# Optimization experiments

Measured on AMD Instinct MI355X. Metric: run time of the kernel, lower is better.

## Reference

```python
import jax, jax.numpy as jnp
import numpy as np

B, L, R, H, TE = 4, 256, 64, 768, 100
TH = 0.5  # all four thresholds default to 0.5


def extract_first_embeddings(tok, start_probs, end_probs, threshold):
    """For each token i with start_prob>th, pair it with the nearest end index j>=i
    with end_prob>th; span embedding = mean(tok[i:j+1]). Valid spans are packed
    (in order) into a [b, l, h] table padded with zeros, with a [b, l] validity mask.
    Vectorized, jit-friendly reconstruction of the repo's span extractor."""
    b, l, h = tok.shape
    ar = jnp.arange(l)
    starts = start_probs > threshold            # [b, l]
    ends = end_probs > threshold                # [b, l]
    end_pos = jnp.where(ends, ar[None, :], l)   # l = sentinel 'no end'
    next_end = jax.lax.cummin(end_pos, axis=1, reverse=True)  # first end >= i
    valid = starts & (next_end < l)             # [b, l]
    j = jnp.minimum(next_end, l - 1)
    # inclusive span mean via prefix sums: mean = (csum[j+1] - csum[i]) / (j-i+1)
    csum0 = jnp.concatenate([jnp.zeros((b, 1, h), tok.dtype), jnp.cumsum(tok, axis=1)], axis=1)
    upper = jnp.take_along_axis(csum0, (j + 1)[:, :, None], axis=1)  # [b, l, h]
    lower = csum0[:, :-1]                                             # csum0[:, i]
    span_len = (j - ar[None, :] + 1).astype(tok.dtype)[:, :, None]
    span_emb = (upper - lower) / span_len
    # pack valid spans to the front (pad_sequence-style), pad with zeros to length l
    rank = jnp.cumsum(valid, axis=1) - 1
    rank_safe = jnp.where(valid, rank, l)       # dump invalids into extra slot l
    padded = jnp.zeros((b, l + 1, h), tok.dtype).at[
        jnp.arange(b)[:, None], rank_safe
    ].set(jnp.where(valid[:, :, None], span_emb, 0.0))[:, :l]
    num = valid.sum(axis=1)
    mask = ar[None, :] < num[:, None]
    return padded, mask


def setup_inputs() -> dict:
    key = jax.random.key(0)
    ks = jax.random.split(key, 12)
    s = 0.02
    return {
        "embs": jax.random.normal(ks[0], (B, L, H), jnp.float32),
        "h_gs": jax.random.normal(ks[1], (B, H), jnp.float32),
        "rel_embs": jax.random.normal(ks[2], (R, H), jnp.float32),
        "rel_transe_embs": jax.random.normal(ks[3], (R, TE), jnp.float32),
        "fc_w": jax.random.normal(ks[4], (8, H), jnp.float32) * s,
        "fc_b": jax.random.normal(ks[5], (8,), jnp.float32) * s,
        "Wm": jax.random.normal(ks[6], (10, H, H), jnp.float32) * s,
        "Wb": jax.random.normal(ks[7], (10, H), jnp.float32) * s,
        "V_w": jax.random.normal(ks[8], (H,), jnp.float32) * s,
        "V_b": jax.random.normal(ks[9], (1,), jnp.float32) * s,
        "rproj_w": jax.random.normal(ks[10], (TE, H), jnp.float32) * s,
        "rproj_b": jax.random.normal(ks[11], (H,), jnp.float32) * s,
    }


def _forward(embs, h_gs, rel_embs, rel_transe_embs, fc_w, fc_b, Wm, Wb, V_w, V_b, rproj_w, rproj_b):
    sig = jax.nn.sigmoid
    b_rel = rel_transe_embs @ rproj_w + rproj_b            # [r, h] r_proj

    # ---- first-stage scalar heads on tokens ----
    f_sub_s = embs @ fc_w[0] + fc_b[0]                     # [b, l]
    f_sub_e = embs @ fc_w[1] + fc_b[1]
    b_obj_s = embs @ fc_w[2] + fc_b[2]
    b_obj_e = embs @ fc_w[3] + fc_b[3]

    f_pad, f_mask = extract_first_embeddings(embs, sig(f_sub_s), sig(f_sub_e), TH)
    b_pad, b_mask = extract_first_embeddings(embs, sig(b_obj_s), sig(b_obj_e), TH)
    f_s_w = (f_pad @ Wm[0] + Wb[0]) * f_mask[:, :, None].astype(embs.dtype)  # f_W_s
    b_o_w = (b_pad @ Wm[1] + Wb[1]) * b_mask[:, :, None].astype(embs.dtype)  # b_W_s

    # ---- relation attention: tanh(W_r rel + W_g hg + W_x tok), broadcast [b,l,r,h] ----
    def rel_attn(rel, iWr, iWg, iWx):
        relp = rel @ Wm[iWr] + Wb[iWr]                     # [r, h]
        hgp = h_gs @ Wm[iWg] + Wb[iWg]                     # [b, h]
        tokp = embs @ Wm[iWx] + Wb[iWx]                    # [b, l, h]
        e = jnp.tanh(tokp[:, :, None, :] + relp[None, None, :, :] + hgp[:, None, None, :])
        v = e @ V_w + V_b                                  # [b, l, r]
        A = jax.nn.softmax(v, axis=1)                      # softmax over tokens
        C = jnp.einsum('blr,blh->brh', A, embs)            # relation context
        return C

    f_C = rel_attn(rel_embs, 2, 3, 4)
    b_C = rel_attn(b_rel, 5, 6, 7)

    # ---- pairwise table heads; Hijk = Hik[:,:,None]+C[:,None]+tok[:,:,None] is linear
    # under the scalar head, so compute logits without materializing [b,l,r,h] ----
    f_Hik = f_s_w + embs @ Wm[8] + Wb[8]                   # [b, l, h] (f_Wx2)
    b_Hik = b_o_w + embs @ Wm[9] + Wb[9]                   # (b_Wx2)

    def pair_logits(Hik, C, i):
        t = (Hik + embs) @ fc_w[i]                         # [b, l]
        return t[:, :, None] + (C @ fc_w[i])[:, None, :] + fc_b[i]  # [b, l, r]

    f_obj_s = pair_logits(f_Hik, f_C, 4)
    f_obj_e = pair_logits(f_Hik, f_C, 5)
    b_sub_s = pair_logits(b_Hik, b_C, 6)
    b_sub_e = pair_logits(b_Hik, b_C, 7)

    # order: forward(sub_s, sub_e, obj_s, obj_e), backward(obj_s, obj_e, sub_s, sub_e)
    return (f_sub_s, f_sub_e, f_obj_s, f_obj_e, b_obj_s, b_obj_e, b_sub_s, b_sub_e)


def reference(embs, h_gs, rel_embs, rel_transe_embs, fc_w, fc_b, Wm, Wb, V_w, V_b, rproj_w, rproj_b):
    return _forward(embs, h_gs, rel_embs, rel_transe_embs, fc_w, fc_b, Wm, Wb, V_w, V_b, rproj_w, rproj_b)
```

## Files before the change

kernel.cpp:

```cpp
#include <hip/hip_runtime.h>
#include <cstddef>

using u16 = unsigned short;
typedef __attribute__((ext_vector_type(8))) short bf16x8;
typedef __attribute__((ext_vector_type(4))) short bf16x4;
typedef __attribute__((ext_vector_type(4))) float f32x4;

constexpr int kB = 4, kL = 256, kR = 64, kH = 768, kTE = 100;
constexpr size_t HH = (size_t)kH * kH;

constexpr size_t OFF_FSS = 0;
constexpr size_t OFF_FSE = OFF_FSS + kB * kL;
constexpr size_t OFF_FOS = OFF_FSE + kB * kL;
constexpr size_t OFF_FOE = OFF_FOS + (size_t)kB * kL * kR;
constexpr size_t OFF_BOS = OFF_FOE + (size_t)kB * kL * kR;
constexpr size_t OFF_BOE = OFF_BOS + kB * kL;
constexpr size_t OFF_BSS = OFF_BOE + kB * kL;
constexpr size_t OFF_BSE = OFF_BSS + (size_t)kB * kL * kR;

constexpr size_t WS_WTALL   = 0;
constexpr size_t WS_EMBSB   = WS_WTALL   + 10 * HH / 2;
constexpr size_t WS_RELEMBB = WS_EMBSB   + (1024 * 768) / 2;
constexpr size_t WS_HGSB    = WS_RELEMBB + (64 * 768) / 2;
constexpr size_t WS_BRELB   = WS_HGSB    + (4 * 768) / 2;
constexpr size_t WS_TOKPB   = WS_BRELB   + (64 * 768) / 2;
constexpr size_t WS_RELPF   = WS_TOKPB   + (2 * 1024 * 768) / 2;
constexpr size_t WS_RELPB   = WS_RELPF   + 64 * 768;
constexpr size_t WS_HGPF    = WS_RELPB   + 64 * 768;
constexpr size_t WS_HGPB    = WS_HGPF    + 4 * 768;
constexpr size_t WS_DD      = WS_HGPB    + 4 * 768;
constexpr size_t WS_DA      = WS_DD      + 4 * 1024;
constexpr size_t WS_DB      = WS_DA      + 4 * 1024;
constexpr size_t WS_UA      = WS_DB      + 4 * 1024;
constexpr size_t WS_UB      = WS_UA      + 4 * 768;
constexpr size_t WS_CC      = WS_UB      + 4 * 768;

__device__ inline float fast_rcp(float x) {
#if __has_builtin(__builtin_amdgcn_rcpf)
    return __builtin_amdgcn_rcpf(x);
#else
    return 1.f / x;
#endif
}
__device__ inline float fast_exp2(float x) {
#if __has_builtin(__builtin_amdgcn_exp2f)
    return __builtin_amdgcn_exp2f(x);
#else
    return __exp2f(x);
#endif
}
__device__ inline u16 f2bf(float x) {
    union { float f; unsigned u; } v; v.f = x;
    unsigned r = v.u + 0x7FFFu + ((v.u >> 16) & 1u);
    return (u16)(r >> 16);
}
__device__ inline float bf2f(u16 x) {
    union { unsigned u; float f; } v; v.u = ((unsigned)x) << 16;
    return v.f;
}

__global__ __launch_bounds__(256) void k_prep_all(
        const float* __restrict__ embs, const float* __restrict__ rel_embs,
        const float* __restrict__ h_gs, const float* __restrict__ rel_transe,
        const float* __restrict__ fc_w, const float* __restrict__ fc_b,
        const float* __restrict__ Wm, const float* __restrict__ Wb,
        const float* __restrict__ rproj_w, const float* __restrict__ rproj_b,
        float* __restrict__ out, u16* __restrict__ embsB,
        u16* __restrict__ relembB, u16* __restrict__ hgsB, u16* __restrict__ brelB,
        u16* __restrict__ WtAll,
        float* __restrict__ uA, float* __restrict__ uB, float* __restrict__ cc,
        float* __restrict__ dd)
{
    __shared__ float sh[64 * 65];
    int bx = blockIdx.x, t = threadIdx.x;
    if (bx < 1024) {
        int tok = bx;
        const float* e = embs + (size_t)tok * kH;
        float s[8] = {0, 0, 0, 0, 0, 0, 0, 0};
        for (int h = t; h < kH; h += 256) {
            float x = e[h];
            embsB[(size_t)tok * kH + h] = f2bf(x);
#pragma unroll
            for (int j = 0; j < 8; j++) s[j] += x * fc_w[j * kH + h];
        }
#pragma unroll
        for (int off = 32; off; off >>= 1)
#pragma unroll
            for (int j = 0; j < 8; j++) s[j] += __shfl_down(s[j], off, 64);
        float(*red)[4] = (float(*)[4])sh;
        int wid = t >> 6;
        if ((t & 63) == 0) {
#pragma unroll
            for (int j = 0; j < 8; j++) red[j][wid] = s[j];
        }
        __syncthreads();
        if (t == 0) {
            float r[8];
#pragma unroll
            for (int j = 0; j < 8; j++) r[j] = red[j][0] + red[j][1] + red[j][2] + red[j][3];
            out[OFF_FSS + tok] = r[0] + fc_b[0];
            out[OFF_FSE + tok] = r[1] + fc_b[1];
            out[OFF_BOS + tok] = r[2] + fc_b[2];
            out[OFF_BOE + tok] = r[3] + fc_b[3];
            dd[0 * 1024 + tok] = r[4];
            dd[1 * 1024 + tok] = r[5];
            dd[2 * 1024 + tok] = r[6];
            dd[3 * 1024 + tok] = r[7];
        }
    } else if (bx < 1888) {
        int px = bx - 1024;
        int mi = 2 + px / 144, tile = px % 144;
        int kt = (tile / 12) * 64, nt = (tile % 12) * 64;
        const float* src = Wm + (size_t)mi * HH;
        u16* dst = WtAll + (size_t)mi * HH;
        float(*tl)[65] = (float(*)[65])sh;
        int r = t >> 2, cq = (t & 3) * 16;
        int row = kt + r;
#pragma unroll
        for (int q = 0; q < 4; q++) {
            float4 v = *(const float4*)(src + (size_t)row * kH + nt + cq + q * 4);
            tl[r][cq + q * 4 + 0] = v.x;
            tl[r][cq + q * 4 + 1] = v.y;
            tl[r][cq + q * 4 + 2] = v.z;
            tl[r][cq + q * 4 + 3] = v.w;
        }
        __syncthreads();
        u16* drow = dst + (size_t)(nt + r) * kH + kt + cq;
#pragma unroll
        for (int j = 0; j < 16; j++) drow[j] = f2bf(tl[cq + j][r]);
    } else if (bx < 2656) {
        int gx = bx - 1888;
        int p = gx / 192;
        int wid = t >> 6, lane = t & 63;
        int row = (gx % 192) * 4 + wid;
        const int wmI[4] = {0, 1, 8, 9};
        const float* W  = Wm + (size_t)wmI[p] * HH + (size_t)row * kH;
        const float* wa = fc_w + (size_t)((p & 1) ? 6 : 4) * kH;
        const float* wb = wa + kH;
        float sa = 0.f, sb = 0.f;
        for (int c = lane; c < kH; c += 64) {
            float wv = W[c];
            sa += wv * wa[c];
            sb += wv * wb[c];
        }
#pragma unroll
        for (int off = 32; off; off >>= 1) {
            sa += __shfl_xor(sa, off, 64);
            sb += __shfl_xor(sb, off, 64);
        }
        if (lane == 0) {
            if (p < 2) {
                uA[(2 * p) * kH + row]     = sa;
                uA[(2 * p + 1) * kH + row] = sb;
            } else {
                int q = p - 2;
                uB[(2 * q) * kH + row]     = sa + wa[row];
                uB[(2 * q + 1) * kH + row] = sb + wb[row];
            }
        }
    } else if (bx < 2720) {
        int r = bx - 2656;
        for (int h = t; h < kH; h += 256) relembB[r * kH + h] = f2bf(rel_embs[r * kH + h]);
    } else if (bx < 2724) {
        int r = bx - 2720;
        for (int h = t; h < kH; h += 256) hgsB[r * kH + h] = f2bf(h_gs[r * kH + h]);
    } else if (bx < 2788) {
        int r = bx - 2724;
        if (t < kTE) sh[t] = rel_transe[r * kTE + t];
        __syncthreads();
        float a0 = rproj_b[t], a1 = rproj_b[t + 256], a2 = rproj_b[t + 512];
        for (int k = 0; k < kTE; k++) {
            float rv = sh[k];
            const float* wr = rproj_w + (size_t)k * kH;
            a0 = fmaf(rv, wr[t], a0);
            a1 = fmaf(rv, wr[t + 256], a1);
            a2 = fmaf(rv, wr[t + 512], a2);
        }
        brelB[r * kH + t]       = f2bf(a0);
        brelB[r * kH + t + 256] = f2bf(a1);
        brelB[r * kH + t + 512] = f2bf(a2);
    } else {
        int j = bx - 2788;
        const int wbI[8] = {0, 0, 1, 1, 8, 8, 9, 9};
        const int fcI[8] = {4, 5, 6, 7, 4, 5, 6, 7};
        const float* wb = Wb + (size_t)wbI[j] * kH;
        const float* w  = fc_w + (size_t)fcI[j] * kH;
        float s = 0.f;
        for (int h = t; h < kH; h += 256) s += wb[h] * w[h];
#pragma unroll
        for (int off = 32; off; off >>= 1) s += __shfl_down(s, off, 64);
        int wid = t >> 6;
        if ((t & 63) == 0) sh[wid] = s;
        __syncthreads();
        if (t == 0) cc[j] = sh[0] + sh[1] + sh[2] + sh[3];
    }
}

struct GemmJob {
    const u16* A; const u16* Wt; const float* bias;
    float* C; u16* Cbf; const float* rowmask;
    int M; int K; int ldc; int coff;
};
struct GemmBatch { GemmJob j[6]; };

__device__ inline int swz(int row, int slot) {
    return row * 64 + ((slot ^ (row & 7)) << 3);
}

__global__ __launch_bounds__(256) void k_dots_gemm(GemmBatch batch,
        const float* __restrict__ embs,
        const float* __restrict__ uA, const float* __restrict__ uB,
        float* __restrict__ dA, float* __restrict__ dB)
{
    __shared__ short Als[2][64 * 64];
    __shared__ short Bls[2][64 * 64];
    int bx = blockIdx.x;
    if (bx < 1024) {
        int tok = bx, t = threadIdx.x;
        const float* e = embs + (size_t)tok * kH;
        float s[8] = {0, 0, 0, 0, 0, 0, 0, 0};
        for (int h = t; h < kH; h += 256) {
            float x = e[h];
#pragma unroll
            for (int j = 0; j < 4; j++) {
                s[j]     += x * uA[j * kH + h];
                s[4 + j] += x * uB[j * kH + h];
            }
        }
#pragma unroll
        for (int off = 32; off; off >>= 1)
#pragma unroll
            for (int j = 0; j < 8; j++) s[j] += __shfl_down(s[j], off, 64);
        float(*red)[4] = (float(*)[4])&Als[0][0];
        int wid = t >> 6;
        if ((t & 63) == 0) {
#pragma unroll
            for (int j = 0; j < 8; j++) red[j][wid] = s[j];
        }
        __syncthreads();
        if (t == 0) {
#pragma unroll
            for (int j = 0; j < 4; j++) {
                dA[j * 1024 + tok] = red[j][0] + red[j][1] + red[j][2] + red[j][3];
                dB[j * 1024 + tok] = red[4 + j][0] + red[4 + j][1] + red[4 + j][2] + red[4 + j][3];
            }
        }
        return;
    }
    int g = bx - 1024;
    int jz, mx, ny;
    if (g < 48)       { jz = g / 12;            mx = 0;              ny = g % 12; }
    else if (g < 240) { jz = 4;                 mx = (g - 48) / 12;  ny = (g - 48) % 12; }
    else              { jz = 5;                 mx = (g - 240) / 12; ny = (g - 240) % 12; }
    GemmJob jb = batch.j[jz];

    int tid = threadIdx.x;
    int m0 = mx * 64;
    int n0 = ny * 64;
    int w = tid >> 6, lane = tid & 63;
    int wm = (w >> 1) * 32, wn = (w & 1) * 32;
    int lrow = lane & 15, lhi = lane >> 4;
    int srow = tid >> 2, sc0 = tid & 3;
    int K = jb.K;
    int T = K >> 6;

    f32x4 zero4 = {0.f, 0.f, 0.f, 0.f};
    f32x4 acc[2][2];
#pragma unroll
    for (int i = 0; i < 2; i++)
#pragma unroll
        for (int j = 0; j < 2; j++) acc[i][j] = zero4;

    bf16x8 pa[2], pb[2];

#define LOADT(k0)                                                                 \
    {                                                                             \
        _Pragma("unroll")                                                         \
        for (int q = 0; q < 2; q++) {                                             \
            bf16x8 va;                                                            \
            _Pragma("unroll") for (int z = 0; z < 8; z++) va[z] = 0;              \
            if (m0 + srow < jb.M)                                                 \
                va = *reinterpret_cast<const bf16x8*>(                            \
                    jb.A + (size_t)(m0 + srow) * K + (k0) + (sc0 + q * 4) * 8);   \
            pa[q] = va;                                                           \
            pb[q] = *reinterpret_cast<const bf16x8*>(                             \
                jb.Wt + (size_t)(n0 + srow) * K + (k0) + (sc0 + q * 4) * 8);      \
        }                                                                         \
    }
#define STORET(buf)                                                               \
    {                                                                             \
        _Pragma("unroll")                                                         \
        for (int q = 0; q < 2; q++) {                                             \
            *reinterpret_cast<bf16x8*>(&Als[buf][swz(srow, sc0 + q * 4)]) = pa[q];\
            *reinterpret_cast<bf16x8*>(&Bls[buf][swz(srow, sc0 + q * 4)]) = pb[q];\
        }                                                                         \
    }

    LOADT(0);
    STORET(0);
    __syncthreads();
    int cur = 0;
    for (int t = 0; t < T; t++) {
        if (t + 1 < T) LOADT((t + 1) << 6);
#pragma unroll
        for (int sub = 0; sub < 2; sub++) {
            bf16x8 af[2], bg[2];
#pragma unroll
            for (int i = 0; i < 2; i++) {
                af[i] = *reinterpret_cast<const bf16x8*>(
                    &Als[cur][swz(wm + i * 16 + lrow, sub * 4 + lhi)]);
                bg[i] = *reinterpret_cast<const bf16x8*>(
                    &Bls[cur][swz(wn + i * 16 + lrow, sub * 4 + lhi)]);
            }
#pragma unroll
            for (int i = 0; i < 2; i++)
#pragma unroll
                for (int j = 0; j < 2; j++)
                    acc[i][j] = __builtin_amdgcn_mfma_f32_16x16x32_bf16(af[i], bg[j], acc[i][j], 0, 0, 0);
        }
        if (t + 1 < T) STORET(cur ^ 1);
        __syncthreads();
        cur ^= 1;
    }
#undef LOADT
#undef STORET

#pragma unroll
    for (int i = 0; i < 2; i++) {
#pragma unroll
        for (int j = 0; j < 2; j++) {
            int n = n0 + wn + j * 16 + lrow;
            float bi = jb.bias[n];
#pragma unroll
            for (int q = 0; q < 4; q++) {
                int m = m0 + wm + i * 16 + lhi * 4 + q;
                if (m < jb.M) {
                    float val = acc[i][j][q] + bi;
                    if (jb.rowmask) val = (jb.rowmask[m] != 0.f) ? val : 0.f;
                    if (jb.C)   jb.C[(size_t)m * jb.ldc + jb.coff + n] = val;
                    if (jb.Cbf) jb.Cbf[(size_t)m * jb.ldc + jb.coff + n] = f2bf(val);
                }
            }
        }
    }
}

__global__ __launch_bounds__(512) void k_score(const u16* __restrict__ tokpB,
        const float* __restrict__ relpf, const float* __restrict__ relpb,
        const float* __restrict__ hgpf, const float* __restrict__ hgpb,
        const float* __restrict__ V_w, const float* __restrict__ V_b,
        const float* __restrict__ dd, const float* __restrict__ dA,
        const float* __restrict__ dB, const float* __restrict__ cc,
        const float* __restrict__ fc_b, float* __restrict__ outp)
{
    constexpr float C = 2.8853900817779268f;
    int idx = blockIdx.x;
    int which = idx >> 8, b = (idx >> 6) & 3, r = idx & 63;
    int tid = threadIdx.x;
    int wid = tid >> 6, lane = tid & 63;
    int h0 = lane * 12;
    const float* relp = (which ? relpb : relpf) + (size_t)r * kH + h0;
    const float* hgp  = (which ? hgpb : hgpf) + (size_t)b * kH + h0;
    const float* vw   = V_w + h0;

    __shared__ float sc[kL];
    __shared__ float red2[2][8];
    __shared__ float PA0[kL], PA1[kL], pv0[kL], pv1[kL];
    __shared__ int warr[4];
    __shared__ int itot[4];
    __shared__ float ftot0[4], ftot1[4];

    float av2[12], w2[12], wsum = 0.f;
#pragma unroll
    for (int j = 0; j < 12; j++) {
        av2[j] = C * (relp[j] + hgp[j]);
        float wv = vw[j];
        w2[j] = -2.f * wv;
        wsum += wv;
    }
    float vb = V_b[0];
    const u16* base = tokpB + ((size_t)which * (kB * kL) + b * kL) * kH + h0;

    int l0 = wid * 32;
    bf16x4 t0 = *reinterpret_cast<const bf16x4*>(base + (size_t)l0 * kH);
    bf16x4 t1 = *reinterpret_cast<const bf16x4*>(base + (size_t)l0 * kH + 4);
    bf16x4 t2 = *reinterpret_cast<const bf16x4*>(base + (size_t)l0 * kH + 8);
    for (int l = l0; l < l0 + 32; l++) {
        bf16x4 n0, n1, n2;
        if (l + 1 < l0 + 32) {
            const u16* nrow = base + (size_t)(l + 1) * kH;
            n0 = *reinterpret_cast<const bf16x4*>(nrow);
            n1 = *reinterpret_cast<const bf16x4*>(nrow + 4);
            n2 = *reinterpret_cast<const bf16x4*>(nrow + 8);
        }
        float acc = wsum;
#pragma unroll
        for (int j = 0; j < 4; j++) {
            float e0 = fast_exp2(fmaf(bf2f((u16)t0[j]), C, av2[j]));
            acc = fmaf(w2[j], fast_rcp(e0 + 1.f), acc);
            float e1 = fast_exp2(fmaf(bf2f((u16)t1[j]), C, av2[4 + j]));
            acc = fmaf(w2[4 + j], fast_rcp(e1 + 1.f), acc);
            float e2 = fast_exp2(fmaf(bf2f((u16)t2[j]), C, av2[8 + j]));
            acc = fmaf(w2[8 + j], fast_rcp(e2 + 1.f), acc);
        }
#pragma unroll
        for (int off = 32; off; off >>= 1) acc += __shfl_xor(acc, off, 64);
        if (lane == 0) sc[l] = acc + vb;
        t0 = n0; t1 = n1; t2 = n2;
    }
    __syncthreads();

    int l = tid & 255;
    bool act = tid < 256;
    float x = act ? sc[l] : -3.4e38f;
    float m = x;
#pragma unroll
    for (int off = 32; off; off >>= 1) m = fmaxf(m, __shfl_xor(m, off, 64));
    if (lane == 0) red2[0][wid] = m;
    __syncthreads();
    m = fmaxf(fmaxf(red2[0][0], red2[0][1]), fmaxf(red2[0][2], red2[0][3]));
    float p = act ? __expf(x - m) : 0.f;
    float s = p;
#pragma unroll
    for (int off = 32; off; off >>= 1) s += __shfl_xor(s, off, 64);
    __syncthreads();
    if (lane == 0) red2[0][wid] = s;
    __syncthreads();
    s = red2[0][0] + red2[0][1] + red2[0][2] + red2[0][3];
    float a = p / s;
    const float* ddA = dd + (size_t)(which ? 2 : 0) * 1024 + b * 256;
    const float* ddB = dd + (size_t)(which ? 3 : 1) * 1024 + b * 256;
    float q0 = act ? a * ddA[l] : 0.f;
    float q1 = act ? a * ddB[l] : 0.f;
#pragma unroll
    for (int off = 32; off; off >>= 1) {
        q0 += __shfl_xor(q0, off, 64);
        q1 += __shfl_xor(q1, off, 64);
    }
    __syncthreads();
    if (lane == 0) { red2[0][wid] = q0; red2[1][wid] = q1; }
    __syncthreads();
    float cv0 = red2[0][0] + red2[0][1] + red2[0][2] + red2[0][3];
    float cv1 = red2[1][0] + red2[1][1] + red2[1][2] + red2[1][3];

    int p0 = which ? 2 : 0, p1 = p0 + 1;
    const float* slog = outp + (which ? OFF_BOS : OFF_FSS) + (size_t)b * kL;
    const float* elog = outp + (which ? OFF_BOE : OFF_FSE) + (size_t)b * kL;
    bool st = false;
    int smv = kL;
    float a0v = 0.f, a1v = 0.f;
    if (act) {
        st = slog[l] > 0.f;
        smv = (elog[l] > 0.f) ? l : kL;
        a0v = dA[(size_t)p0 * 1024 + b * 256 + l];
        a1v = dA[(size_t)p1 * 1024 + b * 256 + l];
    }
    int sv = smv;
#pragma unroll
    for (int off2 = 1; off2 < 64; off2 <<= 1) {
        int o = __shfl_down(sv, off2, 64);
        if (lane + off2 < 64) sv = min(sv, o);
    }
    if (act && lane == 0) warr[wid] = sv;
    __syncthreads();
    int next_end = sv;
    if (act)
        for (int w2 = wid + 1; w2 < 4; w2++) next_end = min(next_end, warr[w2]);
    int validi = (act && st && next_end < kL) ? 1 : 0;
    int px = validi;
    float q0v = a0v, q1v = a1v;
#pragma unroll
    for (int off2 = 1; off2 < 64; off2 <<= 1) {
        int oi = __shfl_up(px, off2, 64);
        float o0 = __shfl_up(q0v, off2, 64);
        float o1 = __shfl_up(q1v, off2, 64);
        if (lane >= off2) { px += oi; q0v += o0; q1v += o1; }
    }
    if (act && lane == 63) { itot[wid] = px; ftot0[wid] = q0v; ftot1[wid] = q1v; }
    __syncthreads();
    if (act) {
        for (int w2 = 0; w2 < wid; w2++) { px += itot[w2]; q0v += ftot0[w2]; q1v += ftot1[w2]; }
        PA0[l] = q0v; PA1[l] = q1v;
        pv0[l] = 0.f; pv1[l] = 0.f;
    }
    __syncthreads();
    if (validi) {
        int j = next_end;
        int rk = px - 1;
        float inv = 1.f / (float)(j - l + 1);
        float lo0 = l ? PA0[l - 1] : 0.f;
        float lo1 = l ? PA1[l - 1] : 0.f;
        pv0[rk] = (PA0[j] - lo0) * inv;
        pv1[rk] = (PA1[j] - lo1) * inv;
    }
    __syncthreads();
    if (act) {
        int num = itot[0] + itot[1] + itot[2] + itot[3];
        float tv0 = ((l < num) ? (pv0[l] + cc[p0]) : 0.f)
                  + dB[(size_t)p0 * 1024 + b * 256 + l] + cc[4 + p0];
        float tv1 = ((l < num) ? (pv1[l] + cc[p1]) : 0.f)
                  + dB[(size_t)p1 * 1024 + b * 256 + l] + cc[4 + p1];
        size_t o0 = which ? OFF_BSS : OFF_FOS;
        size_t o1 = which ? OFF_BSE : OFF_FOE;
        float fb0 = fc_b[which ? 6 : 4], fb1 = fc_b[which ? 7 : 5];
        size_t row = (size_t)(b * kL + l);
        outp[o0 + row * kR + r] = tv0 + cv0 + fb0;
        outp[o1 + row * kR + r] = tv1 + cv1 + fb1;
    }
}

extern "C" void kernel_launch(void* const* d_in, const int* in_sizes, int n_in,
                              void* d_out, int out_size, void* d_ws, size_t ws_size,
                              hipStream_t stream)
{
    const float* embs       = (const float*)d_in[0];
    const float* h_gs       = (const float*)d_in[1];
    const float* rel_embs   = (const float*)d_in[2];
    const float* rel_transe = (const float*)d_in[3];
    const float* fc_w       = (const float*)d_in[4];
    const float* fc_b       = (const float*)d_in[5];
    const float* Wm         = (const float*)d_in[6];
    const float* Wb         = (const float*)d_in[7];
    const float* V_w        = (const float*)d_in[8];
    const float* V_b        = (const float*)d_in[9];
    const float* rproj_w    = (const float*)d_in[10];
    const float* rproj_b    = (const float*)d_in[11];
    float* out = (float*)d_out;
    float* ws  = (float*)d_ws;

    u16* WtAll   = (u16*)(ws + WS_WTALL);
    u16* embsB   = (u16*)(ws + WS_EMBSB);
    u16* relembB = (u16*)(ws + WS_RELEMBB);
    u16* hgsB    = (u16*)(ws + WS_HGSB);
    u16* brelB   = (u16*)(ws + WS_BRELB);
    u16* tokpB   = (u16*)(ws + WS_TOKPB);
    float* relpf = ws + WS_RELPF;
    float* relpb = ws + WS_RELPB;
    float* hgpf  = ws + WS_HGPF;
    float* hgpb  = ws + WS_HGPB;
    float* dd    = ws + WS_DD;
    float* dA    = ws + WS_DA;
    float* dB    = ws + WS_DB;
    float* uA    = ws + WS_UA;
    float* uB    = ws + WS_UB;
    float* cc    = ws + WS_CC;

    k_prep_all<<<2796, 256, 0, stream>>>(embs, rel_embs, h_gs, rel_transe,
        fc_w, fc_b, Wm, Wb, rproj_w, rproj_b,
        out, embsB, relembB, hgsB, brelB, WtAll, uA, uB, cc, dd);

    {
        GemmBatch bt;
        bt.j[0] = { relembB, WtAll + 2 * HH, Wb + 2 * kH, relpf, nullptr, nullptr, kR, kH, kH, 0 };
        bt.j[1] = { hgsB,    WtAll + 3 * HH, Wb + 3 * kH, hgpf,  nullptr, nullptr, kB, kH, kH, 0 };
        bt.j[2] = { hgsB,    WtAll + 6 * HH, Wb + 6 * kH, hgpb,  nullptr, nullptr, kB, kH, kH, 0 };
        bt.j[3] = { brelB,   WtAll + 5 * HH, Wb + 5 * kH, relpb, nullptr, nullptr, kR, kH, kH, 0 };
        bt.j[4] = { embsB,   WtAll + 4 * HH, Wb + 4 * kH, nullptr, tokpB,            nullptr, kB * kL, kH, kH, 0 };
        bt.j[5] = { embsB,   WtAll + 7 * HH, Wb + 7 * kH, nullptr, tokpB + (size_t)kB * kL * kH, nullptr, kB * kL, kH, kH, 0 };
        k_dots_gemm<<<1456, 256, 0, stream>>>(bt, embs, uA, uB, dA, dB);
    }

    k_score<<<512, 512, 0, stream>>>(tokpB, relpf, relpb, hgpf, hgpb, V_w, V_b,
                                     dd, dA, dB, cc, fc_b, out);
}
```

Baseline: 71.21 us.

## Compute span tail once per batch and write pairwise outputs in a final kernel

Measured after the change: 70.77 us. No clear change (-0.6%).

```diff
diff --git a/kernel.cpp b/kernel.cpp
--- a/kernel.cpp
+++ b/kernel.cpp
@@ -34,6 +34,14 @@
 constexpr size_t WS_UA      = WS_DB      + 4 * 1024;
 constexpr size_t WS_UB      = WS_UA      + 4 * 768;
 constexpr size_t WS_CC      = WS_UB      + 4 * 768;
+constexpr size_t WS_C4      = WS_CC      + 8;
+constexpr size_t WS_C5      = WS_C4 + 256;
+constexpr size_t WS_C6      = WS_C5 + 256;
+constexpr size_t WS_C7      = WS_C6 + 256;
+constexpr size_t WS_T4      = WS_C7 + 256;
+constexpr size_t WS_T5      = WS_T4 + 1024;
+constexpr size_t WS_T6      = WS_T5 + 1024;
+constexpr size_t WS_T7      = WS_T6 + 1024;
 
 __device__ inline float fast_rcp(float x) {
 #if __has_builtin(__builtin_amdgcn_rcpf)
@@ -351,7 +359,11 @@
         const float* __restrict__ V_w, const float* __restrict__ V_b,
         const float* __restrict__ dd, const float* __restrict__ dA,
         const float* __restrict__ dB, const float* __restrict__ cc,
-        const float* __restrict__ fc_b, float* __restrict__ outp)
+        const float* __restrict__ logits,
+        float* __restrict__ c4, float* __restrict__ c5,
+        float* __restrict__ c6, float* __restrict__ c7,
+        float* __restrict__ t4, float* __restrict__ t5,
+        float* __restrict__ t6, float* __restrict__ t7)
 {
     constexpr float C = 2.8853900817779268f;
     int idx = blockIdx.x;
@@ -440,12 +452,18 @@
     __syncthreads();
     if (lane == 0) { red2[0][wid] = q0; red2[1][wid] = q1; }
     __syncthreads();
-    float cv0 = red2[0][0] + red2[0][1] + red2[0][2] + red2[0][3];
-    float cv1 = red2[1][0] + red2[1][1] + red2[1][2] + red2[1][3];
-
+    if (tid == 0) {
+        float cv0 = red2[0][0] + red2[0][1] + red2[0][2] + red2[0][3];
+        float cv1 = red2[1][0] + red2[1][1] + red2[1][2] + red2[1][3];
+        int loc = b * kR + r;
+        if (which) { c6[loc] = cv0; c7[loc] = cv1; }
+        else       { c4[loc] = cv0; c5[loc] = cv1; }
+    }
+
+    if (r != 0) return;
     int p0 = which ? 2 : 0, p1 = p0 + 1;
-    const float* slog = outp + (which ? OFF_BOS : OFF_FSS) + (size_t)b * kL;
-    const float* elog = outp + (which ? OFF_BOE : OFF_FSE) + (size_t)b * kL;
+    const float* slog = logits + (which ? OFF_BOS : OFF_FSS) + (size_t)b * kL;
+    const float* elog = logits + (which ? OFF_BOE : OFF_FSE) + (size_t)b * kL;
     bool st = false;
     int smv = kL;
     float a0v = 0.f, a1v = 0.f;
@@ -500,12 +518,28 @@
                   + dB[(size_t)p0 * 1024 + b * 256 + l] + cc[4 + p0];
         float tv1 = ((l < num) ? (pv1[l] + cc[p1]) : 0.f)
                   + dB[(size_t)p1 * 1024 + b * 256 + l] + cc[4 + p1];
-        size_t o0 = which ? OFF_BSS : OFF_FOS;
-        size_t o1 = which ? OFF_BSE : OFF_FOE;
-        float fb0 = fc_b[which ? 6 : 4], fb1 = fc_b[which ? 7 : 5];
-        size_t row = (size_t)(b * kL + l);
-        outp[o0 + row * kR + r] = tv0 + cv0 + fb0;
-        outp[o1 + row * kR + r] = tv1 + cv1 + fb1;
+        if (which) { t6[b * kL + l] = tv0; t7[b * kL + l] = tv1; }
+        else       { t4[b * kL + l] = tv0; t5[b * kL + l] = tv1; }
+    }
+}
+
+__global__ __launch_bounds__(64) void k_final(const float* __restrict__ t4,
+        const float* __restrict__ t5, const float* __restrict__ t6,
+        const float* __restrict__ t7, const float* __restrict__ c4,
+        const float* __restrict__ c5, const float* __restrict__ c6,
+        const float* __restrict__ c7, const float* __restrict__ fc_b,
+        float* __restrict__ out)
+{
+    int which = blockIdx.x >> 10;
+    int t = blockIdx.x & 1023;
+    int b = t >> 8;
+    int r = threadIdx.x;
+    if (!which) {
+        out[OFF_FOS + (size_t)t * kR + r] = t4[t] + c4[b * kR + r] + fc_b[4];
+        out[OFF_FOE + (size_t)t * kR + r] = t5[t] + c5[b * kR + r] + fc_b[5];
+    } else {
+        out[OFF_BSS + (size_t)t * kR + r] = t6[t] + c6[b * kR + r] + fc_b[6];
+        out[OFF_BSE + (size_t)t * kR + r] = t7[t] + c7[b * kR + r] + fc_b[7];
     }
 }
 
@@ -544,6 +578,10 @@
     float* uA    = ws + WS_UA;
     float* uB    = ws + WS_UB;
     float* cc    = ws + WS_CC;
+    float* c4 = ws + WS_C4; float* c5 = ws + WS_C5;
+    float* c6 = ws + WS_C6; float* c7 = ws + WS_C7;
+    float* t4 = ws + WS_T4; float* t5 = ws + WS_T5;
+    float* t6 = ws + WS_T6; float* t7 = ws + WS_T7;
 
     k_prep_all<<<2796, 256, 0, stream>>>(embs, rel_embs, h_gs, rel_transe,
         fc_w, fc_b, Wm, Wb, rproj_w, rproj_b,
@@ -561,5 +599,8 @@
     }
 
     k_score<<<512, 512, 0, stream>>>(tokpB, relpf, relpb, hgpf, hgpb, V_w, V_b,
-                                     dd, dA, dB, cc, fc_b, out);
-}
+                                     dd, dA, dB, cc, out,
+                                     c4, c5, c6, c7, t4, t5, t6, t7);
+
+    k_final<<<2 * kB * kL, 64, 0, stream>>>(t4, t5, t6, t7, c4, c5, c6, c7, fc_b, out);
+}
```
